# Optimization experiments

Measured on AMD Instinct MI355X. Metric: run time of the kernel, lower is better.

Reference implementation:

```python
import jax, jax.numpy as jnp
import numpy as np

H = 1024          # hidden_size
M = 512           # moe_intermediate_size
E = 16            # n_routed_experts
TOP_K = 4         # num_experts_per_tok
N_GROUP = 4
TOPK_GROUP = 2
SCALE = 2.5       # routed_scaling_factor
B, S = 2, 1024


def setup_inputs() -> dict:
    key = jax.random.key(0)
    ks = jax.random.split(key, 9)
    sc_h = 1.0 / np.sqrt(H)
    sc_m = 1.0 / np.sqrt(M)
    return {
        "hidden_states": jax.random.normal(ks[0], (B, S, H), jnp.float32),
        "gate_kernel": jax.random.normal(ks[1], (H, E), jnp.float32) * sc_h,
        "gate_bias": jax.random.normal(ks[2], (E,), jnp.float32) * 0.01,
        "w_gate": jax.random.normal(ks[3], (E, H, M), jnp.float32) * sc_h,
        "w_up": jax.random.normal(ks[4], (E, H, M), jnp.float32) * sc_h,
        "w_down": jax.random.normal(ks[5], (E, M, H), jnp.float32) * sc_m,
        "sw_gate": jax.random.normal(ks[6], (H, 2 * M), jnp.float32) * sc_h,
        "sw_up": jax.random.normal(ks[7], (H, 2 * M), jnp.float32) * sc_h,
        "sw_down": jax.random.normal(ks[8], (2 * M, H), jnp.float32) * (1.0 / np.sqrt(2 * M)),
    }


def _gate(x2d, gate_kernel, gate_bias):
    # x2d: [N, H]
    n = x2d.shape[0]
    logits = jnp.dot(x2d.astype(jnp.float32), gate_kernel.astype(jnp.float32))  # [N, E]
    scores = jax.nn.sigmoid(logits)
    scores_for_choice = scores + gate_bias  # noaux_tc correction bias
    # group-limited top-k: sum of top-2 scores per group
    group_scores = scores_for_choice.reshape(n, N_GROUP, E // N_GROUP)
    top2 = jax.lax.top_k(group_scores, k=2)[0]
    group_sum = jnp.sum(top2, axis=-1)                       # [N, G]
    group_idx = jax.lax.top_k(group_sum, k=TOPK_GROUP)[1]    # [N, topk_group]
    group_mask = jnp.zeros_like(group_sum).at[jnp.arange(n)[:, None], group_idx].set(1.0)
    score_mask = jnp.repeat(group_mask[:, :, None], E // N_GROUP, axis=2).reshape(n, E)
    masked_scores = jnp.where(score_mask > 0, scores_for_choice, 0.0)
    topk_weight, topk_idx = jax.lax.top_k(masked_scores, k=TOP_K)
    # norm_topk_prob
    topk_weight = topk_weight / (jnp.sum(topk_weight, axis=-1, keepdims=True) + 1e-20)
    topk_weight = topk_weight * SCALE
    return topk_idx, topk_weight


def reference(hidden_states, gate_kernel, gate_bias, w_gate, w_up, w_down,
              sw_gate, sw_up, sw_down):
    orig_shape = hidden_states.shape
    x = hidden_states.reshape(-1, orig_shape[-1])  # [N, H]
    topk_idx, topk_weight = _gate(x, gate_kernel, gate_bias)
    # combine weight per (token, expert): sum_k (topk_idx==e) * topk_weight
    onehot = (topk_idx[:, :, None] == jnp.arange(E)[None, None, :]).astype(topk_weight.dtype)
    combine = jnp.einsum('nke,nk->ne', onehot, topk_weight)  # [N, E]
    # dense per-expert MLP (faithful to moe_infer which runs every expert)
    g = jnp.einsum('nh,ehm->enm', x, w_gate)   # [E, N, M]
    u = jnp.einsum('nh,ehm->enm', x, w_up)
    inter = jax.nn.silu(g) * u
    y_e = jnp.einsum('enm,emh->enh', inter, w_down)          # [E, N, H]
    y = jnp.einsum('ne,enh->nh', combine, y_e)               # [N, H]
    # shared-expert path
    shared = jnp.dot(jax.nn.silu(jnp.dot(x, sw_gate)) * jnp.dot(x, sw_up), sw_down)
    return (y + shared).reshape(orig_shape)
```

## Files before the change

kernel.cpp:

```cpp
#include <hip/hip_runtime.h>
#include <hip/hip_bf16.h>
#include <cstdint>

#define HID    1024
#define MID    512
#define NEXP   16
#define NTOKS  2048
#define TOPKE  4
#define RSCALE 2.5f
#define CSTR   16

typedef __attribute__((ext_vector_type(8))) short  bf16x8;
typedef __attribute__((ext_vector_type(8))) ushort u16x8;
typedef __attribute__((ext_vector_type(4))) float  f32x4;

__device__ __forceinline__ ushort f2bf(float f){
  unsigned u = __float_as_uint(f);
  u += 0x7fffu + ((u >> 16) & 1u);
  return (ushort)(u >> 16);
}
__device__ __forceinline__ float bf2f(ushort h){ return __uint_as_float(((unsigned)h) << 16); }

#define GLD16(g, l) __builtin_amdgcn_global_load_lds( \
    (const __attribute__((address_space(1))) unsigned int*)(g), \
    (__attribute__((address_space(3))) unsigned int*)(l), 16, 0, 0)

__global__ __launch_bounds__(256) void k_route(const float* __restrict__ x,
                                               const float* __restrict__ gk,
                                               const float* __restrict__ gb,
                                               int* __restrict__ counts,
                                               int* __restrict__ tidx,
                                               float* __restrict__ tw)
{
  __shared__ float sc[16][16];
  __shared__ int lcnt[NEXP];
  const int tid = threadIdx.x;
  const int tl  = tid >> 4;
  const int e   = tid & 15;
  const int t   = blockIdx.x * 16 + tl;

  float acc = 0.f;
  const float* xr = x + (size_t)t * HID;
  for (int h = 0; h < HID; h += 4){
    f32x4 xv = *reinterpret_cast<const f32x4*>(xr + h);
    acc += xv[0] * gk[(h+0)*NEXP + e];
    acc += xv[1] * gk[(h+1)*NEXP + e];
    acc += xv[2] * gk[(h+2)*NEXP + e];
    acc += xv[3] * gk[(h+3)*NEXP + e];
  }
  sc[tl][e] = 1.f / (1.f + expf(-acc)) + gb[e];
  if (tid < NEXP) lcnt[tid] = 0;
  __syncthreads();

  if (tid < 16){
    const int tt = blockIdx.x * 16 + tid;
    float s4[NEXP];
    #pragma unroll
    for (int i = 0; i < NEXP; ++i) s4[i] = sc[tid][i];
    float gs[4];
    #pragma unroll
    for (int g = 0; g < 4; ++g){
      float m1 = -1e30f, m2 = -1e30f;
      #pragma unroll
      for (int j = 0; j < 4; ++j){
        float v = s4[g*4+j];
        if (v > m1){ m2 = m1; m1 = v; } else if (v > m2){ m2 = v; }
      }
      gs[g] = m1 + m2;
    }
    int g1 = 0;
    for (int g = 1; g < 4; ++g) if (gs[g] > gs[g1]) g1 = g;
    int g2 = -1;
    for (int g = 0; g < 4; ++g){
      if (g == g1) continue;
      if (g2 < 0 || gs[g] > gs[g2]) g2 = g;
    }
    float ms[NEXP];
    #pragma unroll
    for (int i = 0; i < NEXP; ++i){
      int g = i >> 2;
      ms[i] = (g == g1 || g == g2) ? s4[i] : 0.0f;
    }
    bool used[NEXP];
    #pragma unroll
    for (int i = 0; i < NEXP; ++i) used[i] = false;
    int sel[TOPKE]; float val[TOPKE]; float denom = 0.f;
    #pragma unroll
    for (int k = 0; k < TOPKE; ++k){
      int be = -1; float bv = -1e30f;
      for (int i = 0; i < NEXP; ++i){
        if (used[i]) continue;
        if (ms[i] > bv){ bv = ms[i]; be = i; }
      }
      used[be] = true; sel[k] = be; val[k] = bv; denom += bv;
    }
    float inv = RSCALE / (denom + 1e-20f);
    #pragma unroll
    for (int k = 0; k < TOPKE; ++k){
      tidx[tt*TOPKE + k] = sel[k];
      tw  [tt*TOPKE + k] = val[k] * inv;
      atomicAdd(&lcnt[sel[k]], 1);
    }
  }
  __syncthreads();
  if (tid < NEXP && lcnt[tid]) atomicAdd(&counts[tid * CSTR], lcnt[tid]);
}

__global__ __launch_bounds__(256) void k_place(const int* __restrict__ tidx,
                                               const float* __restrict__ tw,
                                               const int* __restrict__ counts,
                                               int* __restrict__ cursor,
                                               int* __restrict__ tlist,
                                               float* __restrict__ wlist,
                                               int* __restrict__ pos)
{
  __shared__ int lcnt[NEXP];
  __shared__ int lbase[NEXP];
  __shared__ int soff[NEXP];
  const int tid = threadIdx.x;
  const int t = blockIdx.x * 256 + tid;
  if (tid < NEXP){
    lcnt[tid] = 0;
    int s = 0;
    for (int i = 0; i < tid; ++i) s += counts[i * CSTR];
    soff[tid] = s;
  }
  __syncthreads();
  int sel[TOPKE]; float w4[TOPKE]; int ls[TOPKE];
  #pragma unroll
  for (int k = 0; k < TOPKE; ++k){
    sel[k] = tidx[t*TOPKE + k];
    w4[k]  = tw[t*TOPKE + k];
    ls[k]  = atomicAdd(&lcnt[sel[k]], 1);
  }
  __syncthreads();
  if (tid < NEXP) lbase[tid] = atomicAdd(&cursor[tid * CSTR], lcnt[tid]);
  __syncthreads();
  #pragma unroll
  for (int k = 0; k < TOPKE; ++k){
    int p = soff[sel[k]] + lbase[sel[k]] + ls[k];
    tlist[p] = t;
    wlist[p] = w4[k];
    pos[t*TOPKE + k] = p;
  }
}

__global__ __launch_bounds__(256) void k_cvt(const float* __restrict__ in,
                                             ushort* __restrict__ out, int n8)
{
  int i = blockIdx.x * 256 + threadIdx.x;
  if (i >= n8) return;
  f32x4 a = *reinterpret_cast<const f32x4*>(in + (size_t)i*8);
  f32x4 b = *reinterpret_cast<const f32x4*>(in + (size_t)i*8 + 4);
  u16x8 o;
  o[0]=f2bf(a[0]); o[1]=f2bf(a[1]); o[2]=f2bf(a[2]); o[3]=f2bf(a[3]);
  o[4]=f2bf(b[0]); o[5]=f2bf(b[1]); o[6]=f2bf(b[2]); o[7]=f2bf(b[3]);
  *reinterpret_cast<u16x8*>(out + (size_t)i*8) = o;
}

__device__ __forceinline__ void tr_body(const float* __restrict__ in,
                                        ushort* __restrict__ out, int K, int N)
{
  const int kb = blockIdx.y * 64, nb = blockIdx.x * 64;
  __shared__ ushort T[64 * 68];
  const int t = threadIdx.x;
  const int r = t >> 4, c4 = (t & 15) * 4;
  #pragma unroll
  for (int i = 0; i < 4; ++i){
    f32x4 v = *reinterpret_cast<const f32x4*>(in + (size_t)(kb + r + i*16) * N + nb + c4);
    #pragma unroll
    for (int j = 0; j < 4; ++j)
      T[(c4 + j) * 68 + r + i*16] = f2bf(v[j]);
  }
  __syncthreads();
  #pragma unroll
  for (int i = 0; i < 4; ++i){
    int n = r + i*16;
    ushort4 o = *reinterpret_cast<const ushort4*>(&T[n * 68 + c4]);
    *reinterpret_cast<ushort4*>(out + (size_t)(nb + n) * K + kb + c4) = o;
  }
}

__global__ __launch_bounds__(256) void k_trS(const float* __restrict__ a,
                                             const float* __restrict__ b,
                                             const float* __restrict__ c,
                                             ushort* __restrict__ oa,
                                             ushort* __restrict__ ob,
                                             ushort* __restrict__ oc)
{
  const int z = blockIdx.z;
  const float* in = (z == 0) ? a : (z == 1) ? b : c;
  ushort* out     = (z == 0) ? oa : (z == 1) ? ob : oc;
  tr_body(in, out, 1024, 1024);
}

__global__ __launch_bounds__(256) void k_trR(const float* __restrict__ a,
                                             const float* __restrict__ b,
                                             ushort* __restrict__ oa,
                                             ushort* __restrict__ ob,
                                             int K, int N, int split)
{
  const int z = blockIdx.z;
  const int e = z % split;
  const float* in = ((z < split) ? a : b) + (size_t)e * K * N;
  ushort* out     = ((z < split) ? oa : ob) + (size_t)e * K * N;
  tr_body(in, out, K, N);
}

__global__ __launch_bounds__(256) void k_mm0(
    const ushort* __restrict__ xb,
    ushort* __restrict__ i_s, ushort* __restrict__ i_r,
    const ushort* __restrict__ swgT, const ushort* __restrict__ swuT,
    const ushort* __restrict__ wgT,  const ushort* __restrict__ wuT,
    const int* __restrict__ counts, const int* __restrict__ tlist)
{
  const int z = blockIdx.z;
  const bool routed = (z >= 2);
  const int e = z - 2;
  const int mbase = blockIdx.y * 128;
  int cnt = NTOKS, aoff = 0;
  if (routed){
    cnt = counts[e * CSTR];
    if (mbase >= cnt) return;
    for (int i = 0; i < e; ++i) aoff += counts[i * CSTR];
  }
  const int N       = routed ? 512 : 1024;
  const int colBase = routed ? (blockIdx.x * 64) : (z * 512 + blockIdx.x * 64);
  const ushort* Bg = routed ? (wgT + (size_t)e * MID * HID) : swgT;
  const ushort* Bu = routed ? (wuT + (size_t)e * MID * HID) : swuT;
  ushort* O = routed ? i_r : i_s;

  __shared__ __align__(16) ushort Sh[16384];

  const int tid = threadIdx.x;
  const int l   = tid & 63;
  const int w   = tid >> 6;
  const int wm  = w >> 1;
  const int wn  = w & 1;

  const int rl     = l >> 3;
  const int srcOff = 8 * ((l & 7) ^ rl);

  const ushort* srcP[8];
  #pragma unroll
  for (int j = 0; j < 8; ++j){
    int g = w * 8 + j;
    const ushort* p;
    if (g < 16){
      int ar = mbase + g * 8 + rl;
      if (routed){
        int s = aoff + (ar < cnt ? ar : cnt - 1);
        p = xb + (size_t)tlist[s] * HID;
      } else p = xb + (size_t)ar * HID;
    } else if (g < 24){
      p = Bg + (size_t)(colBase + (g - 16) * 8 + rl) * HID;
    } else {
      p = Bu + (size_t)(colBase + (g - 24) * 8 + rl) * HID;
    }
    srcP[j] = p + srcOff;
  }

  f32x4 accg[4][2], accu[4][2];
  #pragma unroll
  for (int i = 0; i < 4; ++i)
    #pragma unroll
    for (int j = 0; j < 2; ++j){
      accg[i][j] = (f32x4){0.f,0.f,0.f,0.f};
      accu[i][j] = (f32x4){0.f,0.f,0.f,0.f};
    }

  const int fr  = l & 15;
  const int ko  = l >> 4;
  const int swz = (fr & 7) << 4;

  for (int kt = 0; kt < 16; ++kt){
    const int ke = kt * 64;
    #pragma unroll
    for (int j = 0; j < 8; ++j)
      GLD16(srcP[j] + ke, (ushort*)Sh + (w*8 + j) * 512 + l * 8);
    __syncthreads();
    #pragma unroll
    for (int ks = 0; ks < 2; ++ks){
      const int co = ks * 64 + ko * 16;
      bf16x8 af[4], bg[2], bu[2];
      #pragma unroll
      for (int mf = 0; mf < 4; ++mf)
        af[mf] = *reinterpret_cast<const bf16x8*>(
            (const char*)Sh + (wm*64 + mf*16 + fr) * 128 + (co ^ swz));
      #pragma unroll
      for (int nf = 0; nf < 2; ++nf){
        int cc = wn*32 + nf*16 + fr;
        bg[nf] = *reinterpret_cast<const bf16x8*>(
            (const char*)Sh + 16384 + cc * 128 + (co ^ swz));
        bu[nf] = *reinterpret_cast<const bf16x8*>(
            (const char*)Sh + 24576 + cc * 128 + (co ^ swz));
      }
      #pragma unroll
      for (int mf = 0; mf < 4; ++mf)
        #pragma unroll
        for (int nf = 0; nf < 2; ++nf){
          accg[mf][nf] = __builtin_amdgcn_mfma_f32_16x16x32_bf16(af[mf], bg[nf], accg[mf][nf], 0, 0, 0);
          accu[mf][nf] = __builtin_amdgcn_mfma_f32_16x16x32_bf16(af[mf], bu[nf], accu[mf][nf], 0, 0, 0);
        }
    }
    __syncthreads();
  }

  const int ccol = l & 15;
  const int crow = (l >> 4) * 4;
  #pragma unroll
  for (int mf = 0; mf < 4; ++mf){
    #pragma unroll
    for (int r_ = 0; r_ < 4; ++r_){
      const int arel = wm*64 + mf*16 + crow + r_ + mbase;
      if (routed && arel >= cnt) continue;
      size_t row = routed ? (size_t)(aoff + arel) : (size_t)arel;
      #pragma unroll
      for (int nf = 0; nf < 2; ++nf){
        int col = colBase + wn*32 + nf*16 + ccol;
        float g = accg[mf][nf][r_];
        float u = accu[mf][nf][r_];
        float s = g / (1.f + expf(-g));
        O[row * N + col] = f2bf(s * u);
      }
    }
  }
}

__global__ __launch_bounds__(256) void k_mm1(
    const ushort* __restrict__ i_s, const ushort* __restrict__ i_r,
    const ushort* __restrict__ swdT, const ushort* __restrict__ wdT,
    ushort* __restrict__ y_s, ushort* __restrict__ y_r,
    const int* __restrict__ counts, const float* __restrict__ wlist)
{
  const int z = blockIdx.z;
  const bool routed = (z > 0);
  const int e = z - 1;
  const int Kd = routed ? MID : HID;
  const int mbase = blockIdx.y * 128;
  const int nbase = blockIdx.x * 128;
  int cnt = NTOKS, aoff = 0;
  if (routed){
    cnt = counts[e * CSTR];
    if (mbase >= cnt) return;
    for (int i = 0; i < e; ++i) aoff += counts[i * CSTR];
  }
  const ushort* A = routed ? i_r : i_s;
  const ushort* B = routed ? (wdT + (size_t)e * HID * MID) : swdT;

  __shared__ __align__(16) ushort Sh[16384];

  const int tid = threadIdx.x;
  const int l   = tid & 63;
  const int w   = tid >> 6;
  const int wm  = w >> 1;
  const int wn  = w & 1;

  const int rl     = l >> 3;
  const int srcOff = 8 * ((l & 7) ^ rl);

  const ushort* srcP[8];
  #pragma unroll
  for (int j = 0; j < 8; ++j){
    int g = w * 8 + j;
    const ushort* p;
    if (g < 16){
      int ar = mbase + g * 8 + rl;
      if (routed){
        int s = aoff + (ar < cnt ? ar : cnt - 1);
        p = A + (size_t)s * Kd;
      } else p = A + (size_t)ar * Kd;
    } else {
      p = B + (size_t)(nbase + (g - 16) * 8 + rl) * Kd;
    }
    srcP[j] = p + srcOff;
  }

  f32x4 acc[4][4];
  #pragma unroll
  for (int i = 0; i < 4; ++i)
    #pragma unroll
    for (int j = 0; j < 4; ++j)
      acc[i][j] = (f32x4){0.f,0.f,0.f,0.f};

  const int fr  = l & 15;
  const int ko  = l >> 4;
  const int swz = (fr & 7) << 4;
  const int nk  = Kd >> 6;

  for (int kt = 0; kt < nk; ++kt){
    const int ke = kt * 64;
    #pragma unroll
    for (int j = 0; j < 8; ++j)
      GLD16(srcP[j] + ke, (ushort*)Sh + (w*8 + j) * 512 + l * 8);
    __syncthreads();
    #pragma unroll
    for (int ks = 0; ks < 2; ++ks){
      const int co = ks * 64 + ko * 16;
      bf16x8 af[4], bf[4];
      #pragma unroll
      for (int mf = 0; mf < 4; ++mf)
        af[mf] = *reinterpret_cast<const bf16x8*>(
            (const char*)Sh + (wm*64 + mf*16 + fr) * 128 + (co ^ swz));
      #pragma unroll
      for (int nf = 0; nf < 4; ++nf)
        bf[nf] = *reinterpret_cast<const bf16x8*>(
            (const char*)Sh + 16384 + (wn*64 + nf*16 + fr) * 128 + (co ^ swz));
      #pragma unroll
      for (int mf = 0; mf < 4; ++mf)
        #pragma unroll
        for (int nf = 0; nf < 4; ++nf)
          acc[mf][nf] = __builtin_amdgcn_mfma_f32_16x16x32_bf16(af[mf], bf[nf], acc[mf][nf], 0, 0, 0);
    }
    __syncthreads();
  }

  const int ccol = l & 15;
  const int crow = (l >> 4) * 4;
  #pragma unroll
  for (int mf = 0; mf < 4; ++mf){
    #pragma unroll
    for (int r_ = 0; r_ < 4; ++r_){
      const int arel = wm*64 + mf*16 + crow + r_ + mbase;
      if (routed && arel >= cnt) continue;
      if (!routed){
        #pragma unroll
        for (int nf = 0; nf < 4; ++nf){
          int col = nbase + wn*64 + nf*16 + ccol;
          y_s[(size_t)arel * HID + col] = f2bf(acc[mf][nf][r_]);
        }
      } else {
        int s = aoff + arel;
        float wgt = wlist[s];
        #pragma unroll
        for (int nf = 0; nf < 4; ++nf){
          int col = nbase + wn*64 + nf*16 + ccol;
          y_r[(size_t)s * HID + col] = f2bf(wgt * acc[mf][nf][r_]);
        }
      }
    }
  }
}

__global__ __launch_bounds__(256) void k_comb(const ushort* __restrict__ y_s,
                                              const ushort* __restrict__ y_r,
                                              const int* __restrict__ pos,
                                              float* __restrict__ out)
{
  const int t  = blockIdx.x * 2 + (threadIdx.x >> 7);
  const int c8 = (threadIdx.x & 127) * 8;
  const int* pp = pos + t * TOPKE;
  u16x8 vs = *reinterpret_cast<const u16x8*>(y_s + (size_t)t * HID + c8);
  float s[8];
  #pragma unroll
  for (int j = 0; j < 8; ++j) s[j] = bf2f(vs[j]);
  #pragma unroll
  for (int k = 0; k < TOPKE; ++k){
    int p = pp[k];
    u16x8 vr = *reinterpret_cast<const u16x8*>(y_r + (size_t)p * HID + c8);
    #pragma unroll
    for (int j = 0; j < 8; ++j) s[j] += bf2f(vr[j]);
  }
  f32x4 o0 = (f32x4){s[0],s[1],s[2],s[3]};
  f32x4 o1 = (f32x4){s[4],s[5],s[6],s[7]};
  *reinterpret_cast<f32x4*>(out + (size_t)t * HID + c8)     = o0;
  *reinterpret_cast<f32x4*>(out + (size_t)t * HID + c8 + 4) = o1;
}

extern "C" void kernel_launch(void* const* d_in, const int* in_sizes, int n_in,
                              void* d_out, int out_size, void* d_ws, size_t ws_size,
                              hipStream_t stream)
{
  const float* x   = (const float*)d_in[0];
  const float* gk  = (const float*)d_in[1];
  const float* gb  = (const float*)d_in[2];
  const float* wg  = (const float*)d_in[3];
  const float* wu  = (const float*)d_in[4];
  const float* wd  = (const float*)d_in[5];
  const float* swg = (const float*)d_in[6];
  const float* swu = (const float*)d_in[7];
  const float* swd = (const float*)d_in[8];
  float* out = (float*)d_out;
  char* ws = (char*)d_ws;

  const size_t MB = 1ull << 20;
  int*    counts = (int*)(ws + 0);
  int*    cursor = (int*)(ws + 2048);
  int*    tidx   = (int*)(ws + 8192);
  float*  tw     = (float*)(ws + 49152);
  int*    tlist  = (int*)(ws + 90112);
  float*  wlist  = (float*)(ws + 131072);
  int*    pos    = (int*)(ws + 163840);
  ushort* xb     = (ushort*)(ws + 1*MB);
  ushort* swgT   = (ushort*)(ws + 5*MB);
  ushort* swuT   = (ushort*)(ws + 7*MB);
  ushort* swdT   = (ushort*)(ws + 9*MB);
  ushort* wgT    = (ushort*)(ws + 11*MB);
  ushort* wuT    = (ushort*)(ws + 27*MB);
  ushort* wdT    = (ushort*)(ws + 43*MB);
  ushort* i_s    = (ushort*)(ws + 59*MB);
  ushort* i_r    = (ushort*)(ws + 63*MB);
  ushort* y_r    = (ushort*)(ws + 11*MB);
  ushort* y_s    = (ushort*)(ws + 27*MB);

  hipMemsetAsync(ws, 0, 4096, stream);
  k_route<<<128, 256, 0, stream>>>(x, gk, gb, counts, tidx, tw);
  k_place<<<NTOKS/256, 256, 0, stream>>>(tidx, tw, counts, cursor, tlist, wlist, pos);

  k_cvt<<<1024, 256, 0, stream>>>(x, xb, 262144);
  k_trS<<<dim3(16,16,3),  256, 0, stream>>>(swg, swu, swd, swgT, swuT, swdT);
  k_trR<<<dim3( 8,16,32), 256, 0, stream>>>(wg, wu, wgT, wuT, 1024, 512, 16);
  k_trR<<<dim3(16, 8,16), 256, 0, stream>>>(wd, wd, wdT, wdT, 512, 1024, 16);

  k_mm0<<<dim3(8,16,18), 256, 0, stream>>>(xb, i_s, i_r, swgT, swuT, wgT, wuT,
                                           counts, tlist);
  k_mm1<<<dim3(8,16,17), 256, 0, stream>>>(i_s, i_r, swdT, wdT, y_s, y_r,
                                           counts, wlist);
  k_comb<<<NTOKS/2, 256, 0, stream>>>(y_s, y_r, pos, out);
}
```

Measured before the change: 169.5 us.

## Fuse weight transpose and bf16 conversion into GEMM LDS staging

Drops the three separate transpose/convert kernels that rewrote every fp32 weight matrix into transposed bf16 buffers. The two GEMM kernels now load the fp32 weights directly, convert them to bf16 in registers and write them into the swizzled LDS layout themselves. This avoids a full extra read and write pass over the expert and shared weights plus the extra launches. In exchange, the B operand moves from asynchronous global-to-LDS loads to register-staged loads, and each weight tile is read in fp32 by every M-block, which doubles bytes per reuse.

```diff
diff --git a/kernel.cpp b/kernel.cpp
--- a/kernel.cpp
+++ b/kernel.cpp
@@ -158,60 +158,26 @@
   *reinterpret_cast<u16x8*>(out + (size_t)i*8) = o;
 }
 
-__device__ __forceinline__ void tr_body(const float* __restrict__ in,
-                                        ushort* __restrict__ out, int K, int N)
-{
-  const int kb = blockIdx.y * 64, nb = blockIdx.x * 64;
-  __shared__ ushort T[64 * 68];
-  const int t = threadIdx.x;
-  const int r = t >> 4, c4 = (t & 15) * 4;
+__device__ __forceinline__ void stageB4(const float* __restrict__ p, int ldN,
+                                        char* dstBase, int nloc0, int k4)
+{
+  f32x4 v0 = *reinterpret_cast<const f32x4*>(p);
+  f32x4 v1 = *reinterpret_cast<const f32x4*>(p + ldN);
+  f32x4 v2 = *reinterpret_cast<const f32x4*>(p + 2*ldN);
+  f32x4 v3 = *reinterpret_cast<const f32x4*>(p + 3*ldN);
   #pragma unroll
   for (int i = 0; i < 4; ++i){
-    f32x4 v = *reinterpret_cast<const f32x4*>(in + (size_t)(kb + r + i*16) * N + nb + c4);
-    #pragma unroll
-    for (int j = 0; j < 4; ++j)
-      T[(c4 + j) * 68 + r + i*16] = f2bf(v[j]);
-  }
-  __syncthreads();
-  #pragma unroll
-  for (int i = 0; i < 4; ++i){
-    int n = r + i*16;
-    ushort4 o = *reinterpret_cast<const ushort4*>(&T[n * 68 + c4]);
-    *reinterpret_cast<ushort4*>(out + (size_t)(nb + n) * K + kb + c4) = o;
-  }
-}
-
-__global__ __launch_bounds__(256) void k_trS(const float* __restrict__ a,
-                                             const float* __restrict__ b,
-                                             const float* __restrict__ c,
-                                             ushort* __restrict__ oa,
-                                             ushort* __restrict__ ob,
-                                             ushort* __restrict__ oc)
-{
-  const int z = blockIdx.z;
-  const float* in = (z == 0) ? a : (z == 1) ? b : c;
-  ushort* out     = (z == 0) ? oa : (z == 1) ? ob : oc;
-  tr_body(in, out, 1024, 1024);
-}
-
-__global__ __launch_bounds__(256) void k_trR(const float* __restrict__ a,
-                                             const float* __restrict__ b,
-                                             ushort* __restrict__ oa,
-                                             ushort* __restrict__ ob,
-                                             int K, int N, int split)
-{
-  const int z = blockIdx.z;
-  const int e = z % split;
-  const float* in = ((z < split) ? a : b) + (size_t)e * K * N;
-  ushort* out     = ((z < split) ? oa : ob) + (size_t)e * K * N;
-  tr_body(in, out, K, N);
+    int nloc = nloc0 + i;
+    ushort4 q = make_ushort4(f2bf(v0[i]), f2bf(v1[i]), f2bf(v2[i]), f2bf(v3[i]));
+    *reinterpret_cast<ushort4*>(dstBase + nloc*128 + ((2*k4) ^ ((nloc&7)<<4))) = q;
+  }
 }
 
 __global__ __launch_bounds__(256) void k_mm0(
     const ushort* __restrict__ xb,
     ushort* __restrict__ i_s, ushort* __restrict__ i_r,
-    const ushort* __restrict__ swgT, const ushort* __restrict__ swuT,
-    const ushort* __restrict__ wgT,  const ushort* __restrict__ wuT,
+    const float* __restrict__ swg, const float* __restrict__ swu,
+    const float* __restrict__ wg,  const float* __restrict__ wu,
     const int* __restrict__ counts, const int* __restrict__ tlist)
 {
   const int z = blockIdx.z;
@@ -224,10 +190,11 @@
     if (mbase >= cnt) return;
     for (int i = 0; i < e; ++i) aoff += counts[i * CSTR];
   }
-  const int N       = routed ? 512 : 1024;
+  const int Nout    = routed ? 512 : 1024;
+  const int ldN     = routed ? MID : 1024;
   const int colBase = routed ? (blockIdx.x * 64) : (z * 512 + blockIdx.x * 64);
-  const ushort* Bg = routed ? (wgT + (size_t)e * MID * HID) : swgT;
-  const ushort* Bu = routed ? (wuT + (size_t)e * MID * HID) : swuT;
+  const float* Bg = routed ? (wg + (size_t)e * HID * MID) : swg;
+  const float* Bu = routed ? (wu + (size_t)e * HID * MID) : swu;
   ushort* O = routed ? i_r : i_s;
 
   __shared__ __align__(16) ushort Sh[16384];
@@ -241,24 +208,23 @@
   const int rl     = l >> 3;
   const int srcOff = 8 * ((l & 7) ^ rl);
 
-  const ushort* srcP[8];
-  #pragma unroll
-  for (int j = 0; j < 8; ++j){
-    int g = w * 8 + j;
+  const ushort* aP[4];
+  #pragma unroll
+  for (int j = 0; j < 4; ++j){
+    int g = w * 4 + j;
+    int ar = mbase + g * 8 + rl;
     const ushort* p;
-    if (g < 16){
-      int ar = mbase + g * 8 + rl;
-      if (routed){
-        int s = aoff + (ar < cnt ? ar : cnt - 1);
-        p = xb + (size_t)tlist[s] * HID;
-      } else p = xb + (size_t)ar * HID;
-    } else if (g < 24){
-      p = Bg + (size_t)(colBase + (g - 16) * 8 + rl) * HID;
-    } else {
-      p = Bu + (size_t)(colBase + (g - 24) * 8 + rl) * HID;
-    }
-    srcP[j] = p + srcOff;
-  }
+    if (routed){
+      int s = aoff + (ar < cnt ? ar : cnt - 1);
+      p = xb + (size_t)tlist[s] * HID;
+    } else p = xb + (size_t)ar * HID;
+    aP[j] = p + srcOff;
+  }
+
+  const int k4    = w * 16 + (l >> 4) * 4;
+  const int nloc0 = (l & 15) * 4;
+  const float* gp = Bg + (size_t)k4 * ldN + colBase + nloc0;
+  const float* up = Bu + (size_t)k4 * ldN + colBase + nloc0;
 
   f32x4 accg[4][2], accu[4][2];
   #pragma unroll
@@ -276,8 +242,10 @@
   for (int kt = 0; kt < 16; ++kt){
     const int ke = kt * 64;
     #pragma unroll
-    for (int j = 0; j < 8; ++j)
-      GLD16(srcP[j] + ke, (ushort*)Sh + (w*8 + j) * 512 + l * 8);
+    for (int j = 0; j < 4; ++j)
+      GLD16(aP[j] + ke, (ushort*)Sh + (w*4 + j) * 512);
+    stageB4(gp + (size_t)ke * ldN, ldN, (char*)Sh + 16384, nloc0, k4);
+    stageB4(up + (size_t)ke * ldN, ldN, (char*)Sh + 24576, nloc0, k4);
     __syncthreads();
     #pragma unroll
     for (int ks = 0; ks < 2; ++ks){
@@ -321,7 +289,7 @@
         float g = accg[mf][nf][r_];
         float u = accu[mf][nf][r_];
         float s = g / (1.f + expf(-g));
-        O[row * N + col] = f2bf(s * u);
+        O[row * Nout + col] = f2bf(s * u);
       }
     }
   }
@@ -329,7 +297,7 @@
 
 __global__ __launch_bounds__(256) void k_mm1(
     const ushort* __restrict__ i_s, const ushort* __restrict__ i_r,
-    const ushort* __restrict__ swdT, const ushort* __restrict__ wdT,
+    const float* __restrict__ swd, const float* __restrict__ wd,
     ushort* __restrict__ y_s, ushort* __restrict__ y_r,
     const int* __restrict__ counts, const float* __restrict__ wlist)
 {
@@ -345,8 +313,8 @@
     if (mbase >= cnt) return;
     for (int i = 0; i < e; ++i) aoff += counts[i * CSTR];
   }
-  const ushort* A = routed ? i_r : i_s;
-  const ushort* B = routed ? (wdT + (size_t)e * HID * MID) : swdT;
+  const ushort* A  = routed ? i_r : i_s;
+  const float*  B  = routed ? (wd + (size_t)e * MID * HID) : swd;
 
   __shared__ __align__(16) ushort Sh[16384];
 
@@ -359,22 +327,23 @@
   const int rl     = l >> 3;
   const int srcOff = 8 * ((l & 7) ^ rl);
 
-  const ushort* srcP[8];
-  #pragma unroll
-  for (int j = 0; j < 8; ++j){
-    int g = w * 8 + j;
+  const ushort* aP[4];
+  #pragma unroll
+  for (int j = 0; j < 4; ++j){
+    int g = w * 4 + j;
+    int ar = mbase + g * 8 + rl;
     const ushort* p;
-    if (g < 16){
-      int ar = mbase + g * 8 + rl;
-      if (routed){
-        int s = aoff + (ar < cnt ? ar : cnt - 1);
-        p = A + (size_t)s * Kd;
-      } else p = A + (size_t)ar * Kd;
-    } else {
-      p = B + (size_t)(nbase + (g - 16) * 8 + rl) * Kd;
-    }
-    srcP[j] = p + srcOff;
-  }
+    if (routed){
+      int s = aoff + (ar < cnt ? ar : cnt - 1);
+      p = A + (size_t)s * Kd;
+    } else p = A + (size_t)ar * Kd;
+    aP[j] = p + srcOff;
+  }
+
+  const int k4    = w * 16 + (l >> 4) * 4;
+  const int nloc0 = (l & 15) * 4;
+  const float* bp0 = B + (size_t)k4 * HID + nbase + nloc0;
+  const float* bp1 = bp0 + 64;
 
   f32x4 acc[4][4];
   #pragma unroll
@@ -391,8 +360,10 @@
   for (int kt = 0; kt < nk; ++kt){
     const int ke = kt * 64;
     #pragma unroll
-    for (int j = 0; j < 8; ++j)
-      GLD16(srcP[j] + ke, (ushort*)Sh + (w*8 + j) * 512 + l * 8);
+    for (int j = 0; j < 4; ++j)
+      GLD16(aP[j] + ke, (ushort*)Sh + (w*4 + j) * 512);
+    stageB4(bp0 + (size_t)ke * HID, HID, (char*)Sh + 16384, nloc0,      k4);
+    stageB4(bp1 + (size_t)ke * HID, HID, (char*)Sh + 16384, nloc0 + 64, k4);
     __syncthreads();
     #pragma unroll
     for (int ks = 0; ks < 2; ++ks){
@@ -492,29 +463,19 @@
   float*  wlist  = (float*)(ws + 131072);
   int*    pos    = (int*)(ws + 163840);
   ushort* xb     = (ushort*)(ws + 1*MB);
-  ushort* swgT   = (ushort*)(ws + 5*MB);
-  ushort* swuT   = (ushort*)(ws + 7*MB);
-  ushort* swdT   = (ushort*)(ws + 9*MB);
-  ushort* wgT    = (ushort*)(ws + 11*MB);
-  ushort* wuT    = (ushort*)(ws + 27*MB);
-  ushort* wdT    = (ushort*)(ws + 43*MB);
-  ushort* i_s    = (ushort*)(ws + 59*MB);
-  ushort* i_r    = (ushort*)(ws + 63*MB);
-  ushort* y_r    = (ushort*)(ws + 11*MB);
-  ushort* y_s    = (ushort*)(ws + 27*MB);
+  ushort* i_s    = (ushort*)(ws + 5*MB);
+  ushort* i_r    = (ushort*)(ws + 9*MB);
+  ushort* y_s    = (ushort*)(ws + 17*MB);
+  ushort* y_r    = (ushort*)(ws + 21*MB);
 
   hipMemsetAsync(ws, 0, 4096, stream);
   k_route<<<128, 256, 0, stream>>>(x, gk, gb, counts, tidx, tw);
   k_place<<<NTOKS/256, 256, 0, stream>>>(tidx, tw, counts, cursor, tlist, wlist, pos);
-
   k_cvt<<<1024, 256, 0, stream>>>(x, xb, 262144);
-  k_trS<<<dim3(16,16,3),  256, 0, stream>>>(swg, swu, swd, swgT, swuT, swdT);
-  k_trR<<<dim3( 8,16,32), 256, 0, stream>>>(wg, wu, wgT, wuT, 1024, 512, 16);
-  k_trR<<<dim3(16, 8,16), 256, 0, stream>>>(wd, wd, wdT, wdT, 512, 1024, 16);
-
-  k_mm0<<<dim3(8,16,18), 256, 0, stream>>>(xb, i_s, i_r, swgT, swuT, wgT, wuT,
+
+  k_mm0<<<dim3(8,16,18), 256, 0, stream>>>(xb, i_s, i_r, swg, swu, wg, wu,
                                            counts, tlist);
-  k_mm1<<<dim3(8,16,17), 256, 0, stream>>>(i_s, i_r, swdT, wdT, y_s, y_r,
+  k_mm1<<<dim3(8,16,17), 256, 0, stream>>>(i_s, i_r, swd, wd, y_s, y_r,
                                            counts, wlist);
   k_comb<<<NTOKS/2, 256, 0, stream>>>(y_s, y_r, pos, out);
 }
```

Result: slower. 218.7 us (+29.0%).
